# Kernel tuning notes

Hardware: AMD Instinct MI355X
Metric: run time of the kernel (lower is better)

Reference implementation:

```python
import jax, jax.numpy as jnp
import numpy as np

N_NODES = 100000
N_EDGES = 1600000
N_GRAPHS = 512
NFEAT = 64
HIDDEN = 128
NTARGETS = 16
TIME_DIM = 128
NLAYERS = 3  # conv1 + 2 extra convs


def setup_inputs() -> dict:
    key = jax.random.key(0)
    ks = jax.random.split(key, 12)
    x = jax.random.normal(ks[0], (N_NODES, NFEAT), dtype=jnp.float32)
    edge_index = jax.random.randint(ks[1], (2, N_EDGES), 0, N_NODES, dtype=jnp.int64)
    t_embedding = jax.random.normal(ks[2], (N_NODES, TIME_DIM), dtype=jnp.float32)
    batch = jnp.sort(jax.random.randint(ks[3], (N_NODES,), 0, N_GRAPHS, dtype=jnp.int64))
    s = lambda k, shp, fan_in: jax.random.normal(k, shp, jnp.float32) * (1.0 / np.sqrt(fan_in))
    Wt = s(ks[4], (TIME_DIM, HIDDEN), TIME_DIM)
    bt = jnp.zeros((HIDDEN,), jnp.float32)
    W1 = s(ks[5], (NFEAT, HIDDEN), NFEAT)
    b1 = jnp.zeros((HIDDEN,), jnp.float32)
    Ws = s(ks[6], (NLAYERS - 1, HIDDEN, HIDDEN), HIDDEN)
    bs = jnp.zeros((NLAYERS - 1, HIDDEN), jnp.float32)
    Wo = s(ks[7], (HIDDEN, NTARGETS), HIDDEN)
    bo = jnp.zeros((NTARGETS,), jnp.float32)
    return {"x": x, "edge_index": edge_index, "t_embedding": t_embedding,
            "batch": batch, "Wt": Wt, "bt": bt, "W1": W1, "b1": b1,
            "Ws": Ws, "bs": bs, "Wo": Wo, "bo": bo}


def _gcn_conv(h, src, dst, norm, W, b, n_nodes):
    # PyG GCNConv: h' = scatter_add(norm * (h @ W)[src] -> dst) + b
    h = h @ W                                   # [N, out]
    msg = h[src] * norm[:, None]                # [E+N, out]
    agg = jax.ops.segment_sum(msg, dst, num_segments=n_nodes)
    return agg + b


def reference(x, edge_index, t_embedding, batch, Wt, bt, W1, b1, Ws, bs, Wo, bo):
    n = x.shape[0]
    # add self-loops (static shapes)
    loop = jnp.arange(n, dtype=edge_index.dtype)
    src = jnp.concatenate([edge_index[0], loop])
    dst = jnp.concatenate([edge_index[1], loop])
    # symmetric normalization D^-1/2 (A+I) D^-1/2
    deg = jax.ops.segment_sum(jnp.ones(dst.shape[0], x.dtype), dst, num_segments=n)
    dinv = jnp.where(deg > 0, jax.lax.rsqrt(deg), 0.0)
    norm = dinv[src] * dinv[dst]                # [E+N]

    t_emb = jax.nn.relu(t_embedding @ Wt + bt)  # time_mlp
    h = jax.nn.relu(_gcn_conv(x, src, dst, norm, W1, b1, n)) + t_emb
    for i in range(Ws.shape[0]):
        h = jax.nn.relu(_gcn_conv(h, src, dst, norm, Ws[i], bs[i], n))

    # global mean pool over graphs
    gsum = jax.ops.segment_sum(h, batch, num_segments=N_GRAPHS)
    cnt = jax.ops.segment_sum(jnp.ones(n, h.dtype), batch, num_segments=N_GRAPHS)
    pooled = gsum / jnp.maximum(cnt, 1.0)[:, None]
    return pooled @ Wo + bo
```

## Files before the change

kernel.cpp:

```cpp
#include <hip/hip_runtime.h>

#define N_NODES  100000
#define N_EDGES  1600000
#define N_GRAPHS 512
#define HID      128
#define NB       782
#define NCHUNK   196
#define CHUNK    8192
#define ECAP     512

typedef unsigned int  uint;
typedef unsigned char uchar;
typedef unsigned short ushort;
typedef __attribute__((ext_vector_type(8))) short  short8;
typedef __attribute__((ext_vector_type(4))) float  f32x4;
typedef __attribute__((ext_vector_type(2))) float  f32x2;

__device__ inline float bflo(uint u) { return __uint_as_float(u << 16); }
__device__ inline float bfhi(uint u) { return __uint_as_float(u & 0xffff0000u); }
__device__ inline ushort f2bf(float f) {
    uint u = __float_as_uint(f);
    return (ushort)((u + 0x7fffu + ((u >> 16) & 1u)) >> 16);
}
__device__ inline uint pk(float a, float b) {
    return (uint)f2bf(a) | ((uint)f2bf(b) << 16);
}

__device__ inline void acc16_fp8(uint4 hv, float w, float* a) {
    f32x2 p;
    p = __builtin_amdgcn_cvt_pk_f32_fp8((int)hv.x, false); a[0]  += w * p.x; a[1]  += w * p.y;
    p = __builtin_amdgcn_cvt_pk_f32_fp8((int)hv.x, true);  a[2]  += w * p.x; a[3]  += w * p.y;
    p = __builtin_amdgcn_cvt_pk_f32_fp8((int)hv.y, false); a[4]  += w * p.x; a[5]  += w * p.y;
    p = __builtin_amdgcn_cvt_pk_f32_fp8((int)hv.y, true);  a[6]  += w * p.x; a[7]  += w * p.y;
    p = __builtin_amdgcn_cvt_pk_f32_fp8((int)hv.z, false); a[8]  += w * p.x; a[9]  += w * p.y;
    p = __builtin_amdgcn_cvt_pk_f32_fp8((int)hv.z, true);  a[10] += w * p.x; a[11] += w * p.y;
    p = __builtin_amdgcn_cvt_pk_f32_fp8((int)hv.w, false); a[12] += w * p.x; a[13] += w * p.y;
    p = __builtin_amdgcn_cvt_pk_f32_fp8((int)hv.w, true);  a[14] += w * p.x; a[15] += w * p.y;
}

__global__ __launch_bounds__(256)
void prep_kernel(const float* __restrict__ Wt, const float* __restrict__ W1,
                 const float* __restrict__ Ws, ushort* __restrict__ packed,
                 const int* __restrict__ batch, int* __restrict__ gstart,
                 const float* __restrict__ temb, ushort* __restrict__ tembb,
                 const int* __restrict__ dst, int* __restrict__ chunk_hist,
                 float* __restrict__ pooled) {
    __shared__ int h[NB];
    int b = blockIdx.x;
    int t = threadIdx.x;
    if (b < 224) {
        int tid = b * 256 + t;
        const float* src; int p; ushort* dstp;
        if (tid < 16384)      { src = Wt;         p = tid;         dstp = packed; }
        else if (tid < 24576) { src = W1;         p = tid - 16384; dstp = packed + 16384; }
        else if (tid < 40960) { src = Ws;         p = tid - 24576; dstp = packed + 24576; }
        else                  { src = Ws + 16384; p = tid - 40960; dstp = packed + 40960; }
        int j  = p & 7;
        int L  = (p >> 3) & 63;
        int cb = (p >> 9) & 7;
        int s  = p >> 12;
        int k  = s * 32 + (L >> 4) * 8 + j;
        int n  = cb * 16 + (L & 15);
        dstp[p] = f2bf(src[k * 128 + n]);
    } else if (b < 615) {
        int i = (b - 224) * 256 + t;
        if (i >= N_NODES) return;
        int bb = batch[i];
        int prev = (i == 0) ? -1 : batch[i - 1];
        for (int g = prev + 1; g <= bb; ++g) gstart[g] = i;
        if (i == N_NODES - 1) {
            for (int g = bb + 1; g <= N_GRAPHS; ++g) gstart[g] = N_NODES;
        }
    } else if (b < 3740) {
        long i = ((long)(b - 615) * 256 + t) * 16;
#pragma unroll
        for (int k = 0; k < 4; ++k) {
            float4 f = *(const float4*)(temb + i + k * 4);
            uint2 o; o.x = pk(f.x, f.y); o.y = pk(f.z, f.w);
            *(uint2*)(tembb + i + k * 4) = o;
        }
    } else if (b < 3936) {
        int c = b - 3740;
        for (int i = t; i < NB; i += 256) h[i] = 0;
        __syncthreads();
        const int4* d4 = (const int4*)dst;
#pragma unroll
        for (int k = 0; k < 8; ++k) {
            int i4 = c * (CHUNK / 4) + k * 256 + t;
            if (i4 < N_EDGES / 4) {
                int4 d = d4[i4];
                atomicAdd(&h[d.x >> 7], 1);
                atomicAdd(&h[d.y >> 7], 1);
                atomicAdd(&h[d.z >> 7], 1);
                atomicAdd(&h[d.w >> 7], 1);
            }
        }
        __syncthreads();
        for (int i = t; i < NB; i += 256) chunk_hist[c * NB + i] = h[i];
    } else {
        pooled[(b - 3936) * 256 + t] = 0.f;
    }
}


__global__ __launch_bounds__(256)
void scanA(const int* __restrict__ chunk_hist, int* __restrict__ cbaseT,
           int* __restrict__ btotal) {
    __shared__ int sc[256];
    int b = blockIdx.x, t = threadIdx.x;
    int v = (t < NCHUNK) ? chunk_hist[t * NB + b] : 0;
    sc[t] = v;
    __syncthreads();
    for (int off = 1; off < 256; off <<= 1) {
        int x = (t >= off) ? sc[t - off] : 0;
        __syncthreads();
        sc[t] += x;
        __syncthreads();
    }
    if (t < NCHUNK) cbaseT[b * NCHUNK + t] = sc[t] - v;
    if (t == 255) btotal[b] = sc[255];
}

__global__ __launch_bounds__(256)
void scanB(const int* __restrict__ btotal, int* __restrict__ bstart,
           int* __restrict__ row_ptr) {
    __shared__ int sc[256];
    int t = threadIdx.x;
    int v[4]; int sum = 0;
#pragma unroll
    for (int k = 0; k < 4; ++k) {
        int idx = t * 4 + k;
        v[k] = (idx < NB) ? btotal[idx] : 0;
        sum += v[k];
    }
    sc[t] = sum;
    __syncthreads();
    for (int off = 1; off < 256; off <<= 1) {
        int x = (t >= off) ? sc[t - off] : 0;
        __syncthreads();
        sc[t] += x;
        __syncthreads();
    }
    int run = sc[t] - sum;
#pragma unroll
    for (int k = 0; k < 4; ++k) {
        int idx = t * 4 + k;
        if (idx < NB) bstart[idx] = run;
        run += v[k];
    }
    if (t == 0) { bstart[NB] = N_EDGES; row_ptr[N_NODES] = N_EDGES; }
}

__global__ __launch_bounds__(256)
void scatter_coarse(const int* __restrict__ src, const int* __restrict__ dst,
                    const int* __restrict__ cbaseT, const int* __restrict__ bstart,
                    uint* __restrict__ tmp) {
    __shared__ int cur[NB];
    int c = blockIdx.x, t = threadIdx.x;
    for (int i = t; i < NB; i += 256) cur[i] = cbaseT[i * NCHUNK + c] + bstart[i];
    __syncthreads();
    const int4* s4p = (const int4*)src;
    const int4* d4p = (const int4*)dst;
#pragma unroll
    for (int k = 0; k < 8; ++k) {
        int i4 = c * (CHUNK / 4) + k * 256 + t;
        if (i4 < N_EDGES / 4) {
            int4 s = s4p[i4];
            int4 d = d4p[i4];
            int p;
            p = atomicAdd(&cur[d.x >> 7], 1); tmp[p] = (uint)s.x | (((uint)(d.x & 127)) << 17);
            p = atomicAdd(&cur[d.y >> 7], 1); tmp[p] = (uint)s.y | (((uint)(d.y & 127)) << 17);
            p = atomicAdd(&cur[d.z >> 7], 1); tmp[p] = (uint)s.z | (((uint)(d.z & 127)) << 17);
            p = atomicAdd(&cur[d.w >> 7], 1); tmp[p] = (uint)s.w | (((uint)(d.w & 127)) << 17);
        }
    }
}

__global__ __launch_bounds__(256)
void csr_fine(const uint* __restrict__ tmp, const int* __restrict__ bstart,
              int* __restrict__ row_ptr, float* __restrict__ dinv,
              int* __restrict__ edge, const float* __restrict__ x,
              uchar* __restrict__ xb8) {
    __shared__ int   cnt[128];
    __shared__ float dvloc[128];
    __shared__ int   ps[128];
    int b = blockIdx.x, t = threadIdx.x;
    int node0 = b << 7;
    int ncnt = min(128, N_NODES - node0);
    int s = bstart[b], e = bstart[b + 1];
    if (t < 128) cnt[t] = 0;
    __syncthreads();
    for (int i = s + t; i < e; i += 256) atomicAdd(&cnt[tmp[i] >> 17], 1);
    __syncthreads();
    int c0 = (t < 128) ? cnt[t] : 0;
    if (t < 128) ps[t] = c0;
    __syncthreads();
    for (int off = 1; off < 128; off <<= 1) {
        int v = (t < 128 && t >= off) ? ps[t - off] : 0;
        __syncthreads();
        if (t < 128) ps[t] += v;
        __syncthreads();
    }
    if (t < 128) {
        int p0 = s + ps[t] - c0;
        float dv = rsqrtf((float)(c0 + 1));
        if (t < ncnt) { row_ptr[node0 + t] = p0; dinv[node0 + t] = dv; }
        dvloc[t] = dv;
        cnt[t] = p0;
    }
    __syncthreads();
    for (int i = s + t; i < e; i += 256) {
        uint rec = tmp[i];
        int p = atomicAdd(&cnt[rec >> 17], 1);
        edge[p] = (int)(rec & 0x1FFFFu);
    }
    for (int idx = t; idx < ncnt * 16; idx += 256) {
        int row = idx >> 4, q = idx & 15;
        float4 f = ((const float4*)(x + (size_t)(node0 + row) * 64))[q];
        float d = dvloc[row];
        int w = __builtin_amdgcn_cvt_pk_fp8_f32(f.x * d, f.y * d, 0, false);
        w     = __builtin_amdgcn_cvt_pk_fp8_f32(f.z * d, f.w * d, w, true);
        *(uint*)(xb8 + (size_t)(node0 + row) * 64 + q * 4) = (uint)w;
    }
}

template <int K, bool TEMB, bool OUT8, bool SCALEOUT, bool POOL>
__global__ __launch_bounds__(256)
void fused_conv(const void* __restrict__ Hv, const int* __restrict__ rp,
                const int* __restrict__ edge, const float* __restrict__ dinv,
                const ushort* __restrict__ Wp, const float* __restrict__ bias,
                const ushort* __restrict__ tembb, const ushort* __restrict__ Wtp,
                const float* __restrict__ bias_t, void* __restrict__ Ov,
                const int* __restrict__ batchp, float* __restrict__ pooled, int ntiles) {
    constexpr int LPR  = K / 16;
    constexpr int G    = 64 / LPR;
    constexpr int RPG  = 16 / G;
    constexpr int U    = 8;
    constexpr int LROW = 136;
    __shared__ __align__(16) ushort sA[4][16 * LROW];
    __shared__ uint sE[4][ECAP];
    const int wave = threadIdx.x >> 6;
    const int lane = threadIdx.x & 63;
    const int tile = blockIdx.x * 4 + wave;
    if (tile >= ntiles) return;
    const int row0 = tile * 16;
    const int g  = lane / LPR;
    const int fq = lane % LPR;
    ushort* myA = sA[wave];
    const uchar* H8 = (const uchar*)Hv;

    int   rpv = rp[row0 + ((lane < 17) ? lane : 16)];
    float dvv = dinv[row0 + ((lane < 16) ? lane : 15)];

    const int s0   = __shfl(rpv, 0);
    const int e15  = __shfl(rpv, 16);
    const int ecnt = e15 - s0;
    uint* sEw = sE[wave];
    for (int i = lane; i < ecnt && i < ECAP; i += 64)
        sEw[i] = ((const uint*)edge)[s0 + i];

    auto phase1 = [&](auto eload) {
        for (int rr = 0; rr < RPG; ++rr) {
            int r = g * RPG + rr;
            int v = row0 + r;
            int s = __shfl(rpv, r), e = __shfl(rpv, r + 1);
            float a[16];
            {
                uint4 xv = *(const uint4*)(H8 + (size_t)v * K + fq * 16);
                f32x2 p;
                p = __builtin_amdgcn_cvt_pk_f32_fp8((int)xv.x, false); a[0]  = p.x; a[1]  = p.y;
                p = __builtin_amdgcn_cvt_pk_f32_fp8((int)xv.x, true);  a[2]  = p.x; a[3]  = p.y;
                p = __builtin_amdgcn_cvt_pk_f32_fp8((int)xv.y, false); a[4]  = p.x; a[5]  = p.y;
                p = __builtin_amdgcn_cvt_pk_f32_fp8((int)xv.y, true);  a[6]  = p.x; a[7]  = p.y;
                p = __builtin_amdgcn_cvt_pk_f32_fp8((int)xv.z, false); a[8]  = p.x; a[9]  = p.y;
                p = __builtin_amdgcn_cvt_pk_f32_fp8((int)xv.z, true);  a[10] = p.x; a[11] = p.y;
                p = __builtin_amdgcn_cvt_pk_f32_fp8((int)xv.w, false); a[12] = p.x; a[13] = p.y;
                p = __builtin_amdgcn_cvt_pk_f32_fp8((int)xv.w, true);  a[14] = p.x; a[15] = p.y;
            }
            int iters = (e - s + U - 1) / U;
            int j = s;
            for (int i = 0; i < iters; ++i, j += U) {
                int sv[U];
#pragma unroll
                for (int u = 0; u < U; ++u) {
                    int jv = j + u;
                    int jj = (jv < e) ? jv : e - 1;
                    sv[u] = eload(jj);
                }
                uint4 hv[U];
#pragma unroll
                for (int u = 0; u < U; ++u)
                    hv[u] = *(const uint4*)(H8 + (size_t)sv[u] * K + fq * 16);
#pragma unroll
                for (int u = 0; u < U; ++u) {
                    float w = (j + u < e) ? 1.0f : 0.0f;
                    acc16_fp8(hv[u], w, a);
                }
            }
            float dv = __shfl(dvv, r);
            uint4 o1, o2;
            o1.x = pk(a[0] * dv,  a[1] * dv);  o1.y = pk(a[2] * dv,  a[3] * dv);
            o1.z = pk(a[4] * dv,  a[5] * dv);  o1.w = pk(a[6] * dv,  a[7] * dv);
            o2.x = pk(a[8] * dv,  a[9] * dv);  o2.y = pk(a[10] * dv, a[11] * dv);
            o2.z = pk(a[12] * dv, a[13] * dv); o2.w = pk(a[14] * dv, a[15] * dv);
            *(uint4*)(myA + r * LROW + fq * 16)     = o1;
            *(uint4*)(myA + r * LROW + fq * 16 + 8) = o2;
        }
    };
    if (ecnt <= ECAP) {
        phase1([&](int jj) { return (int)sEw[jj - s0]; });
    } else {
        phase1([&](int jj) { return (int)((const uint*)edge)[jj]; });
    }

    const int m = lane & 15, q = lane >> 4;
    f32x4 acc[8];
#pragma unroll
    for (int cb = 0; cb < 8; ++cb) acc[cb] = {0.f, 0.f, 0.f, 0.f};
    constexpr int S = K / 32;
#pragma unroll
    for (int s = 0; s < S; ++s) {
        short8 av = *(const short8*)(myA + m * LROW + s * 32 + q * 8);
#pragma unroll
        for (int cb = 0; cb < 8; ++cb) {
            short8 b = *(const short8*)(Wp + (size_t)((s * 8 + cb) * 64 + lane) * 8);
            acc[cb] = __builtin_amdgcn_mfma_f32_16x16x32_bf16(av, b, acc[cb], 0, 0, 0);
        }
    }

    f32x4 acc2[TEMB ? 8 : 1];
    if constexpr (TEMB) {
#pragma unroll
        for (int cb = 0; cb < 8; ++cb) acc2[cb] = {0.f, 0.f, 0.f, 0.f};
        const ushort* Arow = tembb + (size_t)(row0 + m) * 128 + q * 8;
#pragma unroll
        for (int s2 = 0; s2 < 4; ++s2) {
            short8 av = *(const short8*)(Arow + s2 * 32);
#pragma unroll
            for (int cb = 0; cb < 8; ++cb) {
                short8 b = *(const short8*)(Wtp + (size_t)((s2 * 8 + cb) * 64 + lane) * 8);
                acc2[cb] = __builtin_amdgcn_mfma_f32_16x16x32_bf16(av, b, acc2[cb], 0, 0, 0);
            }
        }
    }

    float dsc[4];
    if constexpr (SCALEOUT) {
#pragma unroll
        for (int r = 0; r < 4; ++r) dsc[r] = __shfl(dvv, q * 4 + r);
    }
    if constexpr (!OUT8) {
        ushort* Ob = (ushort*)Ov;
#pragma unroll
        for (int cb = 0; cb < 8; ++cb) {
            int colc = cb * 16 + m;
            float bv = bias[colc];
            float bt2 = TEMB ? bias_t[colc] : 0.f;
#pragma unroll
            for (int r = 0; r < 4; ++r) {
                int row = q * 4 + r;
                float v = fmaxf(acc[cb][r] + bv, 0.0f);
                if (TEMB) v += fmaxf(acc2[cb][r] + bt2, 0.0f);
                if (SCALEOUT) v *= dsc[r];
                myA[row * LROW + colc] = f2bf(v);
            }
        }
        if constexpr (!POOL) {
#pragma unroll
            for (int i = 0; i < 4; ++i) {
                int srow = i * 4 + (lane >> 4);
                int scol = (lane & 15) * 8;
                *(short8*)(Ob + (size_t)(row0 + srow) * 128 + scol) =
                    *(const short8*)(myA + srow * LROW + scol);
            }
        } else {
            int gidv = (lane < 16) ? batchp[row0 + lane] : 0;
            int colb = lane * 2;
            float p0 = 0.f, p1 = 0.f;
#pragma unroll
            for (int r = 0; r < 16; ++r) {
                uint u = *(const uint*)(myA + r * LROW + colb);
                p0 += bflo(u); p1 += bfhi(u);
                int curg  = __shfl(gidv, r);
                int nextg = (r < 15) ? __shfl(gidv, r + 1) : -1;
                if (nextg != curg) {
                    atomicAdd(&pooled[curg * 128 + colb],     p0);
                    atomicAdd(&pooled[curg * 128 + colb + 1], p1);
                    p0 = 0.f; p1 = 0.f;
                }
            }
        }
    } else {
        uchar* st8 = (uchar*)myA;
        uchar* Ob = (uchar*)Ov;
#pragma unroll
        for (int cb = 0; cb < 8; ++cb) {
            int colc = cb * 16 + m;
            float bv = bias[colc];
            float bt2 = TEMB ? bias_t[colc] : 0.f;
#pragma unroll
            for (int r = 0; r < 4; ++r) {
                int row = q * 4 + r;
                float v = fmaxf(acc[cb][r] + bv, 0.0f);
                if (TEMB) v += fmaxf(acc2[cb][r] + bt2, 0.0f);
                if (SCALEOUT) v *= dsc[r];
                int enc = __builtin_amdgcn_cvt_pk_fp8_f32(v, v, 0, false);
                st8[row * 136 + colc] = (uchar)(enc & 0xff);
            }
        }
#pragma unroll
        for (int i = 0; i < 4; ++i) {
            int idx = i * 64 + lane;
            int srow = idx >> 4;
            int soff = (idx & 15) * 8;
            *(uint2*)(Ob + (size_t)(row0 + srow) * 128 + soff) =
                *(const uint2*)(st8 + srow * 136 + soff);
        }
    }
}


__global__ __launch_bounds__(256)
void head_kernel(const float* __restrict__ pooled, const int* __restrict__ gstart,
                 const float* __restrict__ Wo, const float* __restrict__ bo,
                 float* __restrict__ out) {
    int g  = blockIdx.x * 16 + (threadIdx.x >> 4);
    int tg = threadIdx.x & 15;
    if (g >= N_GRAPHS) return;
    int c = gstart[g + 1] - gstart[g];
    float inv = 1.0f / (float)(c < 1 ? 1 : c);
    float acc = bo[tg];
    for (int k = 0; k < HID; ++k)
        acc += pooled[g * 128 + k] * inv * Wo[k * 16 + tg];
    out[g * 16 + tg] = acc;
}


extern "C" void kernel_launch(void* const* d_in, const int* in_sizes, int n_in,
                              void* d_out, int out_size, void* d_ws, size_t ws_size,
                              hipStream_t stream) {
    const float* x       = (const float*)d_in[0];
    const int*   ei      = (const int*)d_in[1];
    const float* temb_in = (const float*)d_in[2];
    const int*   batch   = (const int*)d_in[3];
    const float* Wt      = (const float*)d_in[4];
    const float* bt      = (const float*)d_in[5];
    const float* W1      = (const float*)d_in[6];
    const float* b1      = (const float*)d_in[7];
    const float* Ws      = (const float*)d_in[8];
    const float* bs      = (const float*)d_in[9];
    const float* Wo      = (const float*)d_in[10];
    const float* bo      = (const float*)d_in[11];
    float* out = (float*)d_out;

    const int N = N_NODES, E = N_EDGES;
    const int* src = ei;
    const int* dst = ei + E;

    char* p = (char*)d_ws;
    auto carve = [&](size_t bytes) -> void* {
        void* r = (void*)p;
        p += (bytes + 255) & ~(size_t)255;
        return r;
    };
    int*    row_ptr    = (int*)carve((size_t)(N + 1) * 4);
    float*  dinv       = (float*)carve((size_t)N * 4);
    int*    gstart     = (int*)carve((size_t)(N_GRAPHS + 1) * 4);
    ushort* packed     = (ushort*)carve((size_t)57344 * 2);
    int*    chunk_hist = (int*)carve((size_t)NCHUNK * NB * 4);
    int*    cbaseT     = (int*)carve((size_t)NB * NCHUNK * 4);
    int*    btotal     = (int*)carve((size_t)NB * 4);
    int*    bstart     = (int*)carve((size_t)(NB + 1) * 4);
    uint*   tmp        = (uint*)carve((size_t)E * 4);
    int*    edge       = (int*)carve((size_t)E * 4);
    uchar*  xb8        = (uchar*)carve((size_t)(N + 16) * 64);
    ushort* tembb      = (ushort*)carve((size_t)N * 128 * 2);
    uchar*  H1f8       = (uchar*)carve((size_t)(N + 16) * 128);
    uchar*  H2f8       = (uchar*)carve((size_t)(N + 16) * 128);
    float*  pooled     = (float*)carve((size_t)N_GRAPHS * 128 * 4);

    const ushort* Wtp  = packed;
    const ushort* W1p  = packed + 16384;
    const ushort* Ws0p = packed + 24576;
    const ushort* Ws1p = packed + 40960;

    const int ntiles = N / 16;
    const int gblk   = (ntiles + 3) / 4;

    prep_kernel<<<4192, 256, 0, stream>>>(Wt, W1, Ws, packed, batch, gstart,
                                          temb_in, tembb, dst, chunk_hist, pooled);

    scanA<<<NB, 256, 0, stream>>>(chunk_hist, cbaseT, btotal);
    scanB<<<1, 256, 0, stream>>>(btotal, bstart, row_ptr);
    scatter_coarse<<<NCHUNK, 256, 0, stream>>>(src, dst, cbaseT, bstart, tmp);
    csr_fine<<<NB, 256, 0, stream>>>(tmp, bstart, row_ptr, dinv, edge, x, xb8);

    fused_conv<64, true, true, true, false><<<gblk, 256, 0, stream>>>(
        xb8, row_ptr, edge, dinv, W1p, b1, tembb, Wtp, bt, H1f8,
        nullptr, nullptr, ntiles);
    fused_conv<128, false, true, true, false><<<gblk, 256, 0, stream>>>(
        H1f8, row_ptr, edge, dinv, Ws0p, bs, nullptr, nullptr, nullptr, H2f8,
        nullptr, nullptr, ntiles);
    fused_conv<128, false, false, false, true><<<gblk, 256, 0, stream>>>(
        H2f8, row_ptr, edge, dinv, Ws1p, bs + 128, nullptr, nullptr, nullptr, nullptr,
        batch, pooled, ntiles);

    head_kernel<<<32, 256, 0, stream>>>(pooled, gstart, Wo, bo, out);
}
```

Before: 347.1 us.

## Shrink CSR-build chunks, balance rows by degree, split full/tail gather loops

The edge histogram and scatter now use 782 chunks of 2048 edges instead of 196 chunks of 8192, which spreads the CSR build over more blocks. scanA is reworked so each thread scans four chunks. In the fused conv, when each lane group handles two rows, a wave-level bitonic sort by degree pairs heavy rows with light rows to even out per-lane gather work. The aggregation loop is split into an unmasked full-unroll body using packed float2 adds and a masked tail, which removes per-edge weight multiplies. The trade-offs are a larger chunk_hist array and scan, plus sort overhead in every tile.

```diff
diff --git a/kernel.cpp b/kernel.cpp
--- a/kernel.cpp
+++ b/kernel.cpp
@@ -5,8 +5,8 @@
 #define N_GRAPHS 512
 #define HID      128
 #define NB       782
-#define NCHUNK   196
-#define CHUNK    8192
+#define NCHUNK   782
+#define CHUNK    2048
 #define ECAP     512
 
 typedef unsigned int  uint;
@@ -26,16 +26,25 @@
     return (uint)f2bf(a) | ((uint)f2bf(b) << 16);
 }
 
-__device__ inline void acc16_fp8(uint4 hv, float w, float* a) {
-    f32x2 p;
-    p = __builtin_amdgcn_cvt_pk_f32_fp8((int)hv.x, false); a[0]  += w * p.x; a[1]  += w * p.y;
-    p = __builtin_amdgcn_cvt_pk_f32_fp8((int)hv.x, true);  a[2]  += w * p.x; a[3]  += w * p.y;
-    p = __builtin_amdgcn_cvt_pk_f32_fp8((int)hv.y, false); a[4]  += w * p.x; a[5]  += w * p.y;
-    p = __builtin_amdgcn_cvt_pk_f32_fp8((int)hv.y, true);  a[6]  += w * p.x; a[7]  += w * p.y;
-    p = __builtin_amdgcn_cvt_pk_f32_fp8((int)hv.z, false); a[8]  += w * p.x; a[9]  += w * p.y;
-    p = __builtin_amdgcn_cvt_pk_f32_fp8((int)hv.z, true);  a[10] += w * p.x; a[11] += w * p.y;
-    p = __builtin_amdgcn_cvt_pk_f32_fp8((int)hv.w, false); a[12] += w * p.x; a[13] += w * p.y;
-    p = __builtin_amdgcn_cvt_pk_f32_fp8((int)hv.w, true);  a[14] += w * p.x; a[15] += w * p.y;
+__device__ inline void acc16_pk(uint4 hv, f32x2* a) {
+    a[0] += __builtin_amdgcn_cvt_pk_f32_fp8((int)hv.x, false);
+    a[1] += __builtin_amdgcn_cvt_pk_f32_fp8((int)hv.x, true);
+    a[2] += __builtin_amdgcn_cvt_pk_f32_fp8((int)hv.y, false);
+    a[3] += __builtin_amdgcn_cvt_pk_f32_fp8((int)hv.y, true);
+    a[4] += __builtin_amdgcn_cvt_pk_f32_fp8((int)hv.z, false);
+    a[5] += __builtin_amdgcn_cvt_pk_f32_fp8((int)hv.z, true);
+    a[6] += __builtin_amdgcn_cvt_pk_f32_fp8((int)hv.w, false);
+    a[7] += __builtin_amdgcn_cvt_pk_f32_fp8((int)hv.w, true);
+}
+__device__ inline void acc16_w(uint4 hv, float w, f32x2* a) {
+    a[0] += w * __builtin_amdgcn_cvt_pk_f32_fp8((int)hv.x, false);
+    a[1] += w * __builtin_amdgcn_cvt_pk_f32_fp8((int)hv.x, true);
+    a[2] += w * __builtin_amdgcn_cvt_pk_f32_fp8((int)hv.y, false);
+    a[3] += w * __builtin_amdgcn_cvt_pk_f32_fp8((int)hv.y, true);
+    a[4] += w * __builtin_amdgcn_cvt_pk_f32_fp8((int)hv.z, false);
+    a[5] += w * __builtin_amdgcn_cvt_pk_f32_fp8((int)hv.z, true);
+    a[6] += w * __builtin_amdgcn_cvt_pk_f32_fp8((int)hv.w, false);
+    a[7] += w * __builtin_amdgcn_cvt_pk_f32_fp8((int)hv.w, true);
 }
 
 __global__ __launch_bounds__(256)
@@ -79,13 +88,13 @@
             uint2 o; o.x = pk(f.x, f.y); o.y = pk(f.z, f.w);
             *(uint2*)(tembb + i + k * 4) = o;
         }
-    } else if (b < 3936) {
+    } else if (b < 4522) {
         int c = b - 3740;
         for (int i = t; i < NB; i += 256) h[i] = 0;
         __syncthreads();
         const int4* d4 = (const int4*)dst;
 #pragma unroll
-        for (int k = 0; k < 8; ++k) {
+        for (int k = 0; k < 2; ++k) {
             int i4 = c * (CHUNK / 4) + k * 256 + t;
             if (i4 < N_EDGES / 4) {
                 int4 d = d4[i4];
@@ -98,7 +107,7 @@
         __syncthreads();
         for (int i = t; i < NB; i += 256) chunk_hist[c * NB + i] = h[i];
     } else {
-        pooled[(b - 3936) * 256 + t] = 0.f;
+        pooled[(b - 4522) * 256 + t] = 0.f;
     }
 }
 
@@ -108,8 +117,14 @@
            int* __restrict__ btotal) {
     __shared__ int sc[256];
     int b = blockIdx.x, t = threadIdx.x;
-    int v = (t < NCHUNK) ? chunk_hist[t * NB + b] : 0;
-    sc[t] = v;
+    int v[4]; int sum = 0;
+#pragma unroll
+    for (int k = 0; k < 4; ++k) {
+        int c = t * 4 + k;
+        v[k] = (c < NCHUNK) ? chunk_hist[c * NB + b] : 0;
+        sum += v[k];
+    }
+    sc[t] = sum;
     __syncthreads();
     for (int off = 1; off < 256; off <<= 1) {
         int x = (t >= off) ? sc[t - off] : 0;
@@ -117,7 +132,13 @@
         sc[t] += x;
         __syncthreads();
     }
-    if (t < NCHUNK) cbaseT[b * NCHUNK + t] = sc[t] - v;
+    int run = sc[t] - sum;
+#pragma unroll
+    for (int k = 0; k < 4; ++k) {
+        int c = t * 4 + k;
+        if (c < NCHUNK) cbaseT[b * NCHUNK + c] = run;
+        run += v[k];
+    }
     if (t == 255) btotal[b] = sc[255];
 }
 
@@ -162,7 +183,7 @@
     const int4* s4p = (const int4*)src;
     const int4* d4p = (const int4*)dst;
 #pragma unroll
-    for (int k = 0; k < 8; ++k) {
+    for (int k = 0; k < 2; ++k) {
         int i4 = c * (CHUNK / 4) + k * 256 + t;
         if (i4 < N_EDGES / 4) {
             int4 s = s4p[i4];
@@ -259,27 +280,58 @@
     for (int i = lane; i < ecnt && i < ECAP; i += 64)
         sEw[i] = ((const uint*)edge)[s0 + i];
 
+    int rowA = g, rowB = 0;
+    if constexpr (RPG == 2) {
+        int r15  = lane & 15;
+        int degk = __shfl(rpv, r15 + 1) - __shfl(rpv, r15);
+        int key  = degk * 16 + r15;
+#pragma unroll
+        for (int kk = 2; kk <= 16; kk <<= 1) {
+#pragma unroll
+            for (int jm = kk >> 1; jm >= 1; jm >>= 1) {
+                int other = __shfl_xor(key, jm);
+                bool asc = ((lane & kk) == 0);
+                bool keepmin = (((lane & jm) == 0) == asc);
+                int mn = key < other ? key : other;
+                int mx = key < other ? other : key;
+                key = keepmin ? mn : mx;
+            }
+        }
+        rowA = __shfl(key, g) & 15;
+        rowB = __shfl(key, 15 - g) & 15;
+    }
+
     auto phase1 = [&](auto eload) {
         for (int rr = 0; rr < RPG; ++rr) {
-            int r = g * RPG + rr;
+            int r = (RPG == 2) ? (rr == 0 ? rowA : rowB) : g;
             int v = row0 + r;
             int s = __shfl(rpv, r), e = __shfl(rpv, r + 1);
-            float a[16];
+            f32x2 a[8];
             {
                 uint4 xv = *(const uint4*)(H8 + (size_t)v * K + fq * 16);
-                f32x2 p;
-                p = __builtin_amdgcn_cvt_pk_f32_fp8((int)xv.x, false); a[0]  = p.x; a[1]  = p.y;
-                p = __builtin_amdgcn_cvt_pk_f32_fp8((int)xv.x, true);  a[2]  = p.x; a[3]  = p.y;
-                p = __builtin_amdgcn_cvt_pk_f32_fp8((int)xv.y, false); a[4]  = p.x; a[5]  = p.y;
-                p = __builtin_amdgcn_cvt_pk_f32_fp8((int)xv.y, true);  a[6]  = p.x; a[7]  = p.y;
-                p = __builtin_amdgcn_cvt_pk_f32_fp8((int)xv.z, false); a[8]  = p.x; a[9]  = p.y;
-                p = __builtin_amdgcn_cvt_pk_f32_fp8((int)xv.z, true);  a[10] = p.x; a[11] = p.y;
-                p = __builtin_amdgcn_cvt_pk_f32_fp8((int)xv.w, false); a[12] = p.x; a[13] = p.y;
-                p = __builtin_amdgcn_cvt_pk_f32_fp8((int)xv.w, true);  a[14] = p.x; a[15] = p.y;
-            }
-            int iters = (e - s + U - 1) / U;
+                a[0] = __builtin_amdgcn_cvt_pk_f32_fp8((int)xv.x, false);
+                a[1] = __builtin_amdgcn_cvt_pk_f32_fp8((int)xv.x, true);
+                a[2] = __builtin_amdgcn_cvt_pk_f32_fp8((int)xv.y, false);
+                a[3] = __builtin_amdgcn_cvt_pk_f32_fp8((int)xv.y, true);
+                a[4] = __builtin_amdgcn_cvt_pk_f32_fp8((int)xv.z, false);
+                a[5] = __builtin_amdgcn_cvt_pk_f32_fp8((int)xv.z, true);
+                a[6] = __builtin_amdgcn_cvt_pk_f32_fp8((int)xv.w, false);
+                a[7] = __builtin_amdgcn_cvt_pk_f32_fp8((int)xv.w, true);
+            }
+            int nfull = (e - s) / U;
             int j = s;
-            for (int i = 0; i < iters; ++i, j += U) {
+            for (int i = 0; i < nfull; ++i, j += U) {
+                int sv[U];
+#pragma unroll
+                for (int u = 0; u < U; ++u) sv[u] = eload(j + u);
+                uint4 hv[U];
+#pragma unroll
+                for (int u = 0; u < U; ++u)
+                    hv[u] = *(const uint4*)(H8 + (size_t)sv[u] * K + fq * 16);
+#pragma unroll
+                for (int u = 0; u < U; ++u) acc16_pk(hv[u], a);
+            }
+            if (j < e) {
                 int sv[U];
 #pragma unroll
                 for (int u = 0; u < U; ++u) {
@@ -294,15 +346,15 @@
 #pragma unroll
                 for (int u = 0; u < U; ++u) {
                     float w = (j + u < e) ? 1.0f : 0.0f;
-                    acc16_fp8(hv[u], w, a);
+                    acc16_w(hv[u], w, a);
                 }
             }
             float dv = __shfl(dvv, r);
             uint4 o1, o2;
-            o1.x = pk(a[0] * dv,  a[1] * dv);  o1.y = pk(a[2] * dv,  a[3] * dv);
-            o1.z = pk(a[4] * dv,  a[5] * dv);  o1.w = pk(a[6] * dv,  a[7] * dv);
-            o2.x = pk(a[8] * dv,  a[9] * dv);  o2.y = pk(a[10] * dv, a[11] * dv);
-            o2.z = pk(a[12] * dv, a[13] * dv); o2.w = pk(a[14] * dv, a[15] * dv);
+            o1.x = pk(a[0].x * dv, a[0].y * dv); o1.y = pk(a[1].x * dv, a[1].y * dv);
+            o1.z = pk(a[2].x * dv, a[2].y * dv); o1.w = pk(a[3].x * dv, a[3].y * dv);
+            o2.x = pk(a[4].x * dv, a[4].y * dv); o2.y = pk(a[5].x * dv, a[5].y * dv);
+            o2.z = pk(a[6].x * dv, a[6].y * dv); o2.w = pk(a[7].x * dv, a[7].y * dv);
             *(uint4*)(myA + r * LROW + fq * 16)     = o1;
             *(uint4*)(myA + r * LROW + fq * 16 + 8) = o2;
         }
@@ -487,7 +539,7 @@
     const int ntiles = N / 16;
     const int gblk   = (ntiles + 3) / 4;
 
-    prep_kernel<<<4192, 256, 0, stream>>>(Wt, W1, Ws, packed, batch, gstart,
+    prep_kernel<<<4778, 256, 0, stream>>>(Wt, W1, Ws, packed, batch, gstart,
                                           temb_in, tembb, dst, chunk_hist, pooled);
 
     scanA<<<NB, 256, 0, stream>>>(chunk_hist, cbaseT, btotal);
```

Result: faster. 325.8 us (median of 2 runs) (-6.2%).
